# Performance work log

Hardware: AMD Instinct MI355X
Metric: run time of the kernel (lower is better)

## Reference

```python
import jax, jax.numpy as jnp
import numpy as np

# CaMoE_Block MoE dispatch/combine reference.
# Assumptions (undefined submodules in source): RWKV7_TimeMix/att residual omitted
# (h = ln2(x) directly); SparseRWKVFFN experts modeled as RWKV channel-mix FFNs
# y = relu(h @ W1)^2 @ W2; the LinearTransformerExpert (last expert) uses the same
# FFN form with recon_loss = 0; per-expert confidence head conf_e = sigmoid(h @ wc_e + bc_e).
# Faithful parts: winner selection, winning-bid lookup, straight-through scale
# factor conf / (stop_grad(conf) + 1e-6), per-expert compute, scatter-combine, residual.

B, T, C = 4, 2048, 1024
E = 5            # num_rwkv_experts + 1
H = 4 * C        # FFN hidden
LN_EPS = 1e-5


def setup_inputs() -> dict:
    key = jax.random.key(0)
    ks = jax.random.split(key, 8)
    x = jax.random.normal(ks[0], (B, T, C), dtype=jnp.float32)
    winners = jax.random.randint(ks[1], (B, T), 0, E)
    gamma = jnp.ones((C,), jnp.float32)
    beta = jnp.zeros((C,), jnp.float32)
    w1 = jax.random.normal(ks[2], (E, C, H), jnp.float32) * (1.0 / np.sqrt(C))
    w2 = jax.random.normal(ks[3], (E, H, C), jnp.float32) * (1.0 / np.sqrt(H))
    wc = jax.random.normal(ks[4], (E, C), jnp.float32) * (1.0 / np.sqrt(C))
    bc = jnp.zeros((E,), jnp.float32)
    return {"x": x, "winners": winners, "gamma": gamma, "beta": beta,
            "w1": w1, "w2": w2, "wc": wc, "bc": bc}


def _layernorm(x, gamma, beta):
    mu = jnp.mean(x, axis=-1, keepdims=True)
    var = jnp.mean(jnp.square(x - mu), axis=-1, keepdims=True)
    return (x - mu) * jax.lax.rsqrt(var + LN_EPS) * gamma + beta


def reference(x, winners, gamma, beta, w1, w2, wc, bc):
    b, t, c = x.shape
    e = w1.shape[0]
    h = _layernorm(x, gamma, beta)
    hf = h.reshape(-1, c)                     # [N, C]
    win = winners.reshape(-1)                 # [N]

    # per-expert confidences (bids)
    conf = jax.nn.sigmoid(hf @ wc.T + bc)     # [N, E]
    winning_bids = jnp.take_along_axis(conf, win[:, None], axis=1)  # [N, 1]
    scale = winning_bids / (jax.lax.stop_gradient(winning_bids) + 1e-6)

    # dense all-expert FFN (squared-ReLU channel mix), then top-1 select
    k = jnp.square(jax.nn.relu(jnp.einsum('nc,ech->enh', hf, w1)))  # [E, N, H]
    y = jnp.einsum('enh,ehc->enc', k, w2)                            # [E, N, C]
    sel = jax.nn.one_hot(win, e, dtype=y.dtype)                      # [N, E]
    expert_out = jnp.einsum('ne,enc->nc', sel, y)                    # scatter-combine

    out = (expert_out * scale).reshape(b, t, c)
    return x + out
```

## Files before the change

### kernel.cpp

```cpp
#include <hip/hip_runtime.h>
#include <hip/hip_bf16.h>
#include <stdint.h>

#define N_TOK 8192
#define C_DIM 1024
#define H_DIM 4096
#define E_NUM 5
#define LN_EPS 1e-5f
#define NT_MAX 69
#define N_PAD (NT_MAX * 128)

typedef __hip_bfloat16 bf16;
using s8v = __attribute__((ext_vector_type(8))) short;
using f4v = __attribute__((ext_vector_type(4))) float;

__device__ __forceinline__ void async_ld16(const bf16* g, bf16* l) {
    __builtin_amdgcn_global_load_lds(
        (const __attribute__((address_space(1))) void*)g,
        (__attribute__((address_space(3))) void*)l,
        16, 0, 0);
}


__global__ __launch_bounds__(256) void count_kernel(
    const int* __restrict__ win, int* __restrict__ partial)
{
    __shared__ int c[E_NUM];
    if (threadIdx.x < E_NUM) c[threadIdx.x] = 0;
    __syncthreads();
    int n = blockIdx.x * 256 + threadIdx.x;
    atomicAdd(&c[win[n]], 1);
    __syncthreads();
    if (threadIdx.x < E_NUM) partial[blockIdx.x * E_NUM + threadIdx.x] = c[threadIdx.x];
}

__global__ __launch_bounds__(256) void scan_kernel(
    const int* __restrict__ partial, int* __restrict__ meta)
{
    __shared__ int c[E_NUM];
    int t = threadIdx.x;
    if (t < E_NUM) c[t] = 0;
    __syncthreads();
    if (t < 32 * E_NUM) atomicAdd(&c[t % E_NUM], partial[t]);
    __syncthreads();
    if (t == 0) {
        int off = 0;
        for (int e = 0; e < E_NUM; ++e) {
            meta[e] = c[e];
            meta[5 + e] = off;
            off += (c[e] + 127) & ~127;
            meta[11 + e] = 0;
        }
        meta[10] = off;
        int ti = 0;
        for (int e = 0; e < E_NUM; ++e) {
            int tiles = (c[e] + 127) >> 7;
            for (int j = 0; j < tiles; ++j) meta[16 + ti++] = e;
        }
        for (; ti < NT_MAX; ++ti) meta[16 + ti] = -1;
    }
}

__global__ __launch_bounds__(256) void scatter_kernel(
    const int* __restrict__ win, int* __restrict__ meta,
    int* __restrict__ idx, int* __restrict__ pos)
{
    __shared__ int c[E_NUM];
    __shared__ int base[E_NUM];
    if (threadIdx.x < E_NUM) c[threadIdx.x] = 0;
    __syncthreads();
    int n = blockIdx.x * 256 + threadIdx.x;
    int e = win[n];
    int lr = atomicAdd(&c[e], 1);
    __syncthreads();
    if (threadIdx.x < E_NUM)
        base[threadIdx.x] = atomicAdd(&meta[11 + threadIdx.x], c[threadIdx.x]);
    __syncthreads();
    int p = meta[5 + e] + base[e] + lr;
    idx[p] = n;
    pos[n] = p;
}

__global__ __launch_bounds__(256) void ln_conf_kernel(
    const float* __restrict__ x, const int* __restrict__ win,
    const float* __restrict__ gamma, const float* __restrict__ beta,
    const float* __restrict__ wc, const float* __restrict__ bc,
    const int* __restrict__ pos,
    bf16* __restrict__ hbuf, float* __restrict__ scl)
{
    int n = blockIdx.x;
    int t = threadIdx.x;
    const float* xr = x + (size_t)n * C_DIM;
    float v[4];
    float s = 0.f, ss = 0.f;
#pragma unroll
    for (int i = 0; i < 4; ++i) {
        v[i] = xr[t + i * 256];
        s += v[i];
        ss += v[i] * v[i];
    }
#pragma unroll
    for (int off = 32; off > 0; off >>= 1) {
        s  += __shfl_down(s, off);
        ss += __shfl_down(ss, off);
    }
    __shared__ float red[8];
    __shared__ float mu_s, rv_s;
    int wave = t >> 6, lane = t & 63;
    if (lane == 0) { red[wave] = s; red[4 + wave] = ss; }
    __syncthreads();
    if (t == 0) {
        float S  = red[0] + red[1] + red[2] + red[3];
        float SS = red[4] + red[5] + red[6] + red[7];
        float mu = S * (1.f / C_DIM);
        float var = SS * (1.f / C_DIM) - mu * mu;
        mu_s = mu;
        rv_s = rsqrtf(var + LN_EPS);
    }
    __syncthreads();
    float mu = mu_s, rv = rv_s;
    int e = win[n];
    int p = pos[n];
    const float* wce = wc + (size_t)e * C_DIM;
    float dot = 0.f;
#pragma unroll
    for (int i = 0; i < 4; ++i) {
        int ci = t + i * 256;
        float hv = (v[i] - mu) * rv * gamma[ci] + beta[ci];
        hbuf[(size_t)p * C_DIM + ci] = (bf16)hv;
        dot += hv * wce[ci];
    }
#pragma unroll
    for (int off = 32; off > 0; off >>= 1) dot += __shfl_down(dot, off);
    if (lane == 0) red[wave] = dot;
    __syncthreads();
    if (t == 0) {
        float z = red[0] + red[1] + red[2] + red[3] + bc[e];
        float conf = 1.f / (1.f + expf(-z));
        scl[p] = conf / (conf + 1e-6f);
    }
}

__global__ __launch_bounds__(256) void transpose_cvt_kernel(
    const float* __restrict__ w1, const float* __restrict__ w2,
    bf16* __restrict__ w1t, bf16* __restrict__ w2t)
{
    int bid = blockIdx.x;
    int m = bid >= 5120;
    int r = m ? bid - 5120 : bid;
    int e = r >> 10;
    int cell = r & 1023;
    const float* src; bf16* dst; int R, S, sx, ry;
    if (!m) { src = w1; dst = w1t; R = C_DIM; S = H_DIM; sx = cell & 63; ry = cell >> 6; }
    else    { src = w2; dst = w2t; R = H_DIM; S = C_DIM; sx = cell & 15; ry = cell >> 4; }

    __shared__ float tile[64][65];
    size_t ebase = (size_t)e * (size_t)R * (size_t)S;
    int s0 = sx * 64;
    int r0 = ry * 64;
    int t = threadIdx.x;
    int lr = t >> 4;
    int lc = (t & 15) * 4;
#pragma unroll
    for (int i = 0; i < 4; ++i) {
        int rr = lr + i * 16;
        float4 v = *(const float4*)(src + ebase + (size_t)(r0 + rr) * S + s0 + lc);
        tile[rr][lc + 0] = v.x;
        tile[rr][lc + 1] = v.y;
        tile[rr][lc + 2] = v.z;
        tile[rr][lc + 3] = v.w;
    }
    __syncthreads();
    int ch = t & 7;
    int scb = t >> 3;
#pragma unroll
    for (int p = 0; p < 2; ++p) {
        int sc = scb + p * 32;
        bf16 vals[8];
#pragma unroll
        for (int j = 0; j < 8; ++j)
            vals[j] = (bf16)tile[ch * 8 + j][sc];
        *(s8v*)(dst + ebase + (size_t)(s0 + sc) * R + r0 + ch * 8) = *(s8v*)vals;
    }
}


__global__ __launch_bounds__(256) void gemm1_kernel(
    const bf16* __restrict__ hbuf, const bf16* __restrict__ w1t,
    const int* __restrict__ meta, bf16* __restrict__ ks)
{
    const int GX = H_DIM / 128;
    const int NWG = GX * NT_MAX;
    int d = blockIdx.y * GX + blockIdx.x;
    int w = (d & 7) * (NWG >> 3) + (d >> 3);
    int bx = w & (GX - 1);
    int ti = w / GX;
    int e = meta[16 + ti];
    if (e < 0) return;

    int base_p = meta[5 + e];
    int cnt = meta[e];
    int m0 = ti * 128 - base_p;
    int n0 = bx * 128;

    __shared__ __align__(16) bf16 As[128 * 32];
    __shared__ __align__(16) bf16 Bs[128 * 32];

    int t = threadIdx.x;
    int lane = t & 63;
    int wv = t >> 6;
    int wr = wv >> 1, wcol = wv & 1;

    int i0 = (t & 7) ^ ((t >> 3) & 7);
    int srow = 2 * (t >> 3) + (i0 >> 2);
    int schk = i0 & 3;

    int r1 = min(m0 + srow, cnt - 1);
    int r2 = min(m0 + 64 + srow, cnt - 1);
    const bf16* ga1 = hbuf + (size_t)(base_p + r1) * C_DIM + schk * 8;
    const bf16* ga2 = hbuf + (size_t)(base_p + r2) * C_DIM + schk * 8;
    const bf16* wbase = w1t + (size_t)e * H_DIM * C_DIM;
    const bf16* gb1 = wbase + (size_t)(n0 + srow) * C_DIM + schk * 8;
    const bf16* gb2 = wbase + (size_t)(n0 + 64 + srow) * C_DIM + schk * 8;

    bf16* la1 = As + t * 8;
    bf16* la2 = As + 2048 + t * 8;
    bf16* lb1 = Bs + t * 8;
    bf16* lb2 = Bs + 2048 + t * 8;

    int kq = lane >> 4;
    int rhalf = (lane & 15) >> 1;
    int ifrag = ((lane & 1) << 2) | kq;
    int foff = rhalf * 64 + (ifrag ^ rhalf) * 8;
    const bf16* Af = As + wr * 2048 + foff;
    const bf16* Bf = Bs + wcol * 2048 + foff;

    f4v acc[4][4];
    f4v zero = {0.f, 0.f, 0.f, 0.f};
#pragma unroll
    for (int i = 0; i < 4; ++i)
#pragma unroll
        for (int j = 0; j < 4; ++j) acc[i][j] = zero;

    for (int kb = 0; kb < C_DIM / 32; ++kb) {
        __syncthreads();
        async_ld16(ga1, la1); ga1 += 32;
        async_ld16(ga2, la2); ga2 += 32;
        async_ld16(gb1, lb1); gb1 += 32;
        async_ld16(gb2, lb2); gb2 += 32;
        __syncthreads();
        s8v af[4], bfv[4];
#pragma unroll
        for (int mi = 0; mi < 4; ++mi)
            af[mi] = *(const s8v*)(Af + mi * 512);
#pragma unroll
        for (int ni = 0; ni < 4; ++ni)
            bfv[ni] = *(const s8v*)(Bf + ni * 512);
#pragma unroll
        for (int mi = 0; mi < 4; ++mi)
#pragma unroll
            for (int ni = 0; ni < 4; ++ni)
                acc[mi][ni] = __builtin_amdgcn_mfma_f32_16x16x32_bf16(af[mi], bfv[ni], acc[mi][ni], 0, 0, 0);
    }

#pragma unroll
    for (int mi = 0; mi < 4; ++mi) {
#pragma unroll
        for (int r = 0; r < 4; ++r) {
            int row_local = wr * 64 + mi * 16 + ((lane >> 4) << 2) + r;
            int gm = m0 + row_local;
            if (gm < cnt) {
                size_t p = (size_t)(base_p + gm);
#pragma unroll
                for (int ni = 0; ni < 4; ++ni) {
                    int col = n0 + wcol * 64 + ni * 16 + (lane & 15);
                    float v = acc[mi][ni][r];
                    float rl = fmaxf(v, 0.f);
                    ks[p * H_DIM + col] = (bf16)(rl * rl);
                }
            }
        }
    }
}

__global__ __launch_bounds__(256) void gemm2_kernel(
    const bf16* __restrict__ ks, const bf16* __restrict__ w2t,
    const int* __restrict__ idx, const int* __restrict__ meta,
    const float* __restrict__ x, const float* __restrict__ scl,
    float* __restrict__ out)
{
    const int GX = C_DIM / 128;
    const int NWG = GX * NT_MAX;
    int d = blockIdx.y * GX + blockIdx.x;
    int w = (d & 7) * (NWG >> 3) + (d >> 3);
    int bx = w & (GX - 1);
    int ti = w / GX;
    int e = meta[16 + ti];
    if (e < 0) return;

    int base_p = meta[5 + e];
    int cnt = meta[e];
    int m0 = ti * 128 - base_p;
    int n0 = bx * 128;

    __shared__ __align__(16) bf16 As[3][128 * 32];
    __shared__ __align__(16) bf16 Bs[3][128 * 32];

    int t = threadIdx.x;
    int lane = t & 63;
    int wv = t >> 6;
    int wr = wv >> 1, wcol = wv & 1;

    int i0 = (t & 7) ^ ((t >> 3) & 7);
    int srow = 2 * (t >> 3) + (i0 >> 2);
    int schk = i0 & 3;

    int r1 = min(m0 + srow, cnt - 1);
    int r2 = min(m0 + 64 + srow, cnt - 1);
    const bf16* ga1 = ks + (size_t)(base_p + r1) * H_DIM + schk * 8;
    const bf16* ga2 = ks + (size_t)(base_p + r2) * H_DIM + schk * 8;
    const bf16* wbase = w2t + (size_t)e * C_DIM * H_DIM;
    const bf16* gb1 = wbase + (size_t)(n0 + srow) * H_DIM + schk * 8;
    const bf16* gb2 = wbase + (size_t)(n0 + 64 + srow) * H_DIM + schk * 8;

    int lo1 = t * 8;
    int lo2 = 2048 + t * 8;

    int kq = lane >> 4;
    int rhalf = (lane & 15) >> 1;
    int ifrag = ((lane & 1) << 2) | kq;
    int foff = rhalf * 64 + (ifrag ^ rhalf) * 8;
    int aoff = wr * 2048 + foff;
    int boff = wcol * 2048 + foff;

    f4v acc[4][4];
    f4v zero = {0.f, 0.f, 0.f, 0.f};
#pragma unroll
    for (int i = 0; i < 4; ++i)
#pragma unroll
        for (int j = 0; j < 4; ++j) acc[i][j] = zero;

    const int nk = H_DIM / 32;

#pragma unroll
    for (int pt = 0; pt < 2; ++pt) {
        async_ld16(ga1, &As[pt][lo1]); ga1 += 32;
        async_ld16(ga2, &As[pt][lo2]); ga2 += 32;
        async_ld16(gb1, &Bs[pt][lo1]); gb1 += 32;
        async_ld16(gb2, &Bs[pt][lo2]); gb2 += 32;
    }

    int cur = 0, st = 2;
    for (int kb = 0; kb < nk; ++kb) {
        if (kb < nk - 2) {
            async_ld16(ga1, &As[st][lo1]); ga1 += 32;
            async_ld16(ga2, &As[st][lo2]); ga2 += 32;
            async_ld16(gb1, &Bs[st][lo1]); gb1 += 32;
            async_ld16(gb2, &Bs[st][lo2]); gb2 += 32;
            asm volatile("s_waitcnt vmcnt(8)" ::: "memory");
        } else if (kb == nk - 2) {
            asm volatile("s_waitcnt vmcnt(4)" ::: "memory");
        } else {
            asm volatile("s_waitcnt vmcnt(0)" ::: "memory");
        }
        __builtin_amdgcn_s_barrier();

        const bf16* Ac = &As[cur][0];
        const bf16* Bc = &Bs[cur][0];
        s8v af[4], bfv[4];
#pragma unroll
        for (int mi = 0; mi < 4; ++mi)
            af[mi] = *(const s8v*)(Ac + aoff + mi * 512);
#pragma unroll
        for (int ni = 0; ni < 4; ++ni)
            bfv[ni] = *(const s8v*)(Bc + boff + ni * 512);
#pragma unroll
        for (int mi = 0; mi < 4; ++mi)
#pragma unroll
            for (int ni = 0; ni < 4; ++ni)
                acc[mi][ni] = __builtin_amdgcn_mfma_f32_16x16x32_bf16(af[mi], bfv[ni], acc[mi][ni], 0, 0, 0);

        asm volatile("s_waitcnt lgkmcnt(0)" ::: "memory");
        __builtin_amdgcn_s_barrier();
        cur = (cur == 2) ? 0 : cur + 1;
        st  = (st  == 2) ? 0 : st  + 1;
    }

#pragma unroll
    for (int mi = 0; mi < 4; ++mi) {
        int tok[4];
        float sclv[4];
#pragma unroll
        for (int r = 0; r < 4; ++r) {
            int row_local = wr * 64 + mi * 16 + ((lane >> 4) << 2) + r;
            int gm = m0 + row_local;
            if (gm < cnt) {
                tok[r] = idx[base_p + gm];
                sclv[r] = scl[base_p + gm];
            } else {
                tok[r] = -1;
                sclv[r] = 0.f;
            }
        }
#pragma unroll
        for (int ni = 0; ni < 4; ++ni) {
            int col = n0 + wcol * 64 + ni * 16 + (lane & 15);
#pragma unroll
            for (int r = 0; r < 4; ++r) {
                if (tok[r] >= 0) {
                    size_t o = (size_t)tok[r] * C_DIM + col;
                    out[o] = x[o] + acc[mi][ni][r] * sclv[r];
                }
            }
        }
    }
}

extern "C" void kernel_launch(void* const* d_in, const int* in_sizes, int n_in,
                              void* d_out, int out_size, void* d_ws, size_t ws_size,
                              hipStream_t stream) {
    const float* x     = (const float*)d_in[0];
    const int*   win   = (const int*)d_in[1];
    const float* gamma = (const float*)d_in[2];
    const float* beta  = (const float*)d_in[3];
    const float* w1    = (const float*)d_in[4];
    const float* w2    = (const float*)d_in[5];
    const float* wc    = (const float*)d_in[6];
    const float* bc    = (const float*)d_in[7];
    float* out = (float*)d_out;

    char* ws = (char*)d_ws;
    size_t o = 0;
    bf16* w1t  = (bf16*)(ws + o); o += (size_t)E_NUM * H_DIM * C_DIM * 2;
    bf16* w2t  = (bf16*)(ws + o); o += (size_t)E_NUM * C_DIM * H_DIM * 2;
    bf16* hbuf = (bf16*)(ws + o); o += (size_t)N_PAD * C_DIM * 2;
    bf16* ks   = (bf16*)(ws + o); o += (size_t)N_PAD * H_DIM * 2;
    float* scl = (float*)(ws + o); o += (size_t)N_PAD * 4;
    int* idx   = (int*)(ws + o);   o += (size_t)N_PAD * 4;
    int* pos   = (int*)(ws + o);   o += (size_t)N_TOK * 4;
    int* meta  = (int*)(ws + o);   o += 512;
    int* partial = (int*)(ws + o); o += 32 * E_NUM * 4;

    hipLaunchKernelGGL(count_kernel, dim3(N_TOK / 256), dim3(256), 0, stream, win, partial);
    hipLaunchKernelGGL(scan_kernel, dim3(1), dim3(256), 0, stream, partial, meta);
    hipLaunchKernelGGL(scatter_kernel, dim3(N_TOK / 256), dim3(256), 0, stream, win, meta, idx, pos);
    hipLaunchKernelGGL(transpose_cvt_kernel, dim3(10240), dim3(256), 0, stream,
                       w1, w2, w1t, w2t);
    hipLaunchKernelGGL(ln_conf_kernel, dim3(N_TOK), dim3(256), 0, stream,
                       x, win, gamma, beta, wc, bc, pos, hbuf, scl);
    hipLaunchKernelGGL(gemm1_kernel, dim3(H_DIM / 128, NT_MAX), dim3(256), 0, stream,
                       hbuf, w1t, meta, ks);
    hipLaunchKernelGGL(gemm2_kernel, dim3(C_DIM / 128, NT_MAX), dim3(256), 0, stream,
                       ks, w2t, idx, meta, x, scl, out);
}
```

Before: 441.5 us.

## Fuse weight transposes into LN and GEMM1 launches, merge count and scan

```diff
diff --git a/kernel.cpp b/kernel.cpp
--- a/kernel.cpp
+++ b/kernel.cpp
@@ -22,26 +22,14 @@
 }
 
 
-__global__ __launch_bounds__(256) void count_kernel(
-    const int* __restrict__ win, int* __restrict__ partial)
-{
-    __shared__ int c[E_NUM];
-    if (threadIdx.x < E_NUM) c[threadIdx.x] = 0;
-    __syncthreads();
-    int n = blockIdx.x * 256 + threadIdx.x;
-    atomicAdd(&c[win[n]], 1);
-    __syncthreads();
-    if (threadIdx.x < E_NUM) partial[blockIdx.x * E_NUM + threadIdx.x] = c[threadIdx.x];
-}
-
-__global__ __launch_bounds__(256) void scan_kernel(
-    const int* __restrict__ partial, int* __restrict__ meta)
+__global__ __launch_bounds__(1024) void count_scan_kernel(
+    const int* __restrict__ win, int* __restrict__ meta)
 {
     __shared__ int c[E_NUM];
     int t = threadIdx.x;
     if (t < E_NUM) c[t] = 0;
     __syncthreads();
-    if (t < 32 * E_NUM) atomicAdd(&c[t % E_NUM], partial[t]);
+    for (int n = t; n < N_TOK; n += 1024) atomicAdd(&c[win[n]], 1);
     __syncthreads();
     if (t == 0) {
         int off = 0;
@@ -81,13 +69,53 @@
     pos[n] = p;
 }
 
-__global__ __launch_bounds__(256) void ln_conf_kernel(
+__device__ __forceinline__ void transpose_tile(
+    const float* __restrict__ src, bf16* __restrict__ dst,
+    size_t ebase, int R, int S, int r0, int s0, float (*tile)[65])
+{
+    int t = threadIdx.x;
+    int lr = t >> 4;
+    int lc = (t & 15) * 4;
+#pragma unroll
+    for (int i = 0; i < 4; ++i) {
+        int rr = lr + i * 16;
+        float4 v = *(const float4*)(src + ebase + (size_t)(r0 + rr) * S + s0 + lc);
+        tile[rr][lc + 0] = v.x;
+        tile[rr][lc + 1] = v.y;
+        tile[rr][lc + 2] = v.z;
+        tile[rr][lc + 3] = v.w;
+    }
+    __syncthreads();
+    int ch = t & 7;
+    int scb = t >> 3;
+#pragma unroll
+    for (int p = 0; p < 2; ++p) {
+        int sc = scb + p * 32;
+        bf16 vals[8];
+#pragma unroll
+        for (int j = 0; j < 8; ++j)
+            vals[j] = (bf16)tile[ch * 8 + j][sc];
+        *(s8v*)(dst + ebase + (size_t)(s0 + sc) * R + r0 + ch * 8) = *(s8v*)vals;
+    }
+}
+
+__global__ __launch_bounds__(256) void ln_conf_w1t_kernel(
     const float* __restrict__ x, const int* __restrict__ win,
     const float* __restrict__ gamma, const float* __restrict__ beta,
     const float* __restrict__ wc, const float* __restrict__ bc,
     const int* __restrict__ pos,
-    bf16* __restrict__ hbuf, float* __restrict__ scl)
-{
+    bf16* __restrict__ hbuf, float* __restrict__ scl,
+    const float* __restrict__ w1, bf16* __restrict__ w1t)
+{
+    __shared__ float tile[64][65];
+    if (blockIdx.x >= N_TOK) {
+        int r = blockIdx.x - N_TOK;
+        int e = r >> 10;
+        int cell = r & 1023;
+        transpose_tile(w1, w1t, (size_t)e * C_DIM * H_DIM, C_DIM, H_DIM,
+                       (cell >> 6) * 64, (cell & 63) * 64, tile);
+        return;
+    }
     int n = blockIdx.x;
     int t = threadIdx.x;
     const float* xr = x + (size_t)n * C_DIM;
@@ -141,57 +169,24 @@
     }
 }
 
-__global__ __launch_bounds__(256) void transpose_cvt_kernel(
-    const float* __restrict__ w1, const float* __restrict__ w2,
-    bf16* __restrict__ w1t, bf16* __restrict__ w2t)
-{
-    int bid = blockIdx.x;
-    int m = bid >= 5120;
-    int r = m ? bid - 5120 : bid;
-    int e = r >> 10;
-    int cell = r & 1023;
-    const float* src; bf16* dst; int R, S, sx, ry;
-    if (!m) { src = w1; dst = w1t; R = C_DIM; S = H_DIM; sx = cell & 63; ry = cell >> 6; }
-    else    { src = w2; dst = w2t; R = H_DIM; S = C_DIM; sx = cell & 15; ry = cell >> 4; }
-
-    __shared__ float tile[64][65];
-    size_t ebase = (size_t)e * (size_t)R * (size_t)S;
-    int s0 = sx * 64;
-    int r0 = ry * 64;
-    int t = threadIdx.x;
-    int lr = t >> 4;
-    int lc = (t & 15) * 4;
-#pragma unroll
-    for (int i = 0; i < 4; ++i) {
-        int rr = lr + i * 16;
-        float4 v = *(const float4*)(src + ebase + (size_t)(r0 + rr) * S + s0 + lc);
-        tile[rr][lc + 0] = v.x;
-        tile[rr][lc + 1] = v.y;
-        tile[rr][lc + 2] = v.z;
-        tile[rr][lc + 3] = v.w;
-    }
-    __syncthreads();
-    int ch = t & 7;
-    int scb = t >> 3;
-#pragma unroll
-    for (int p = 0; p < 2; ++p) {
-        int sc = scb + p * 32;
-        bf16 vals[8];
-#pragma unroll
-        for (int j = 0; j < 8; ++j)
-            vals[j] = (bf16)tile[ch * 8 + j][sc];
-        *(s8v*)(dst + ebase + (size_t)(s0 + sc) * R + r0 + ch * 8) = *(s8v*)vals;
-    }
-}
-
-
-__global__ __launch_bounds__(256) void gemm1_kernel(
+
+__global__ __launch_bounds__(256) void gemm1_w2t_kernel(
     const bf16* __restrict__ hbuf, const bf16* __restrict__ w1t,
-    const int* __restrict__ meta, bf16* __restrict__ ks)
+    const int* __restrict__ meta, bf16* __restrict__ ks,
+    const float* __restrict__ w2, bf16* __restrict__ w2t)
 {
     const int GX = H_DIM / 128;
     const int NWG = GX * NT_MAX;
-    int d = blockIdx.y * GX + blockIdx.x;
+    if (blockIdx.x >= NWG) {
+        __shared__ float tile[64][65];
+        int r = blockIdx.x - NWG;
+        int e = r >> 10;
+        int cell = r & 1023;
+        transpose_tile(w2, w2t, (size_t)e * H_DIM * C_DIM, H_DIM, C_DIM,
+                       (cell >> 4) * 64, (cell & 15) * 64, tile);
+        return;
+    }
+    int d = blockIdx.x;
     int w = (d & 7) * (NWG >> 3) + (d >> 3);
     int bx = w & (GX - 1);
     int ti = w / GX;
@@ -439,17 +434,13 @@
     int* idx   = (int*)(ws + o);   o += (size_t)N_PAD * 4;
     int* pos   = (int*)(ws + o);   o += (size_t)N_TOK * 4;
     int* meta  = (int*)(ws + o);   o += 512;
-    int* partial = (int*)(ws + o); o += 32 * E_NUM * 4;
-
-    hipLaunchKernelGGL(count_kernel, dim3(N_TOK / 256), dim3(256), 0, stream, win, partial);
-    hipLaunchKernelGGL(scan_kernel, dim3(1), dim3(256), 0, stream, partial, meta);
+
+    hipLaunchKernelGGL(count_scan_kernel, dim3(1), dim3(1024), 0, stream, win, meta);
     hipLaunchKernelGGL(scatter_kernel, dim3(N_TOK / 256), dim3(256), 0, stream, win, meta, idx, pos);
-    hipLaunchKernelGGL(transpose_cvt_kernel, dim3(10240), dim3(256), 0, stream,
-                       w1, w2, w1t, w2t);
-    hipLaunchKernelGGL(ln_conf_kernel, dim3(N_TOK), dim3(256), 0, stream,
-                       x, win, gamma, beta, wc, bc, pos, hbuf, scl);
-    hipLaunchKernelGGL(gemm1_kernel, dim3(H_DIM / 128, NT_MAX), dim3(256), 0, stream,
-                       hbuf, w1t, meta, ks);
+    hipLaunchKernelGGL(ln_conf_w1t_kernel, dim3(N_TOK + 5120), dim3(256), 0, stream,
+                       x, win, gamma, beta, wc, bc, pos, hbuf, scl, w1, w1t);
+    hipLaunchKernelGGL(gemm1_w2t_kernel, dim3(2208 + 5120), dim3(256), 0, stream,
+                       hbuf, w1t, meta, ks, w2, w2t);
     hipLaunchKernelGGL(gemm2_kernel, dim3(C_DIM / 128, NT_MAX), dim3(256), 0, stream,
                        ks, w2t, idx, meta, x, scl, out);
 }
```

Result: no change. 438.0 us, median of 3 (-0.8%).
